# Optimization experiments

Hardware: AMD Instinct MI355X
Metric: run time of the kernel (lower is better)

Reference implementation:

```python
import jax, jax.numpy as jnp
import numpy as np

N_HEAD = 16


def setup_inputs() -> dict:
    key = jax.random.key(0)
    ks = jax.random.split(key, 5)
    B, T, C = 4, 2048, 1024
    s = 0.02
    x = jax.random.normal(ks[0], (B, T, C), jnp.float32)
    wq = jax.random.normal(ks[1], (C, C), jnp.float32) * s
    wk = jax.random.normal(ks[2], (C, C), jnp.float32) * s
    wv = jax.random.normal(ks[3], (C, C), jnp.float32) * s
    wp = jax.random.normal(ks[4], (C, C), jnp.float32) * s
    zb = jnp.zeros((C,), jnp.float32)
    return {"x": x, "wq": wq, "bq": zb, "wk": wk, "bk": zb,
            "wv": wv, "bv": zb, "wp": wp, "bp": zb}


def _rope_cos_sin(T, D):
    half = D // 2
    i = jnp.arange(half, dtype=jnp.float32)
    alpha = 1.0 / (10000.0 ** (2.0 * i / D))        # [half]
    ang = jnp.arange(T, dtype=jnp.float32)[:, None] * alpha  # [T, half]
    return jnp.cos(ang), jnp.sin(ang)


def _apply_rope(t, cos, sin):
    # t: [B, H, T, D]; non-interleaved halves as in the torch module
    half = t.shape[-1] // 2
    xr, xi = t[..., :half], t[..., half:]
    return jnp.concatenate([xr * cos - xi * sin, xr * sin + xi * cos], axis=-1)


def reference(x, wq, bq, wk, bk, wv, bv, wp, bp):
    B, T, C = x.shape
    H = N_HEAD
    D = C // H
    # QKV projections (torch Linear: x @ W.T + b)
    def heads(w, b):
        return (x @ w.T + b).reshape(B, T, H, D).transpose(0, 2, 1, 3)
    q, k, v = heads(wq, bq), heads(wk, bk), heads(wv, bv)
    cos, sin = _rope_cos_sin(T, D)  # each [T, D//2], broadcasts over B,H
    q = _apply_rope(q, cos, sin)
    k = _apply_rope(k, cos, sin)
    scale = 1.0 / np.sqrt(D).astype(np.float32)
    att = jnp.einsum('bhtd,bhsd->bhts', q, k) * scale  # [B,H,T,T]
    causal = jnp.tril(jnp.ones((T, T), bool))
    att = jnp.where(causal, att, jnp.float32(-jnp.inf))
    att = jax.nn.softmax(att, axis=-1)
    y = jnp.einsum('bhts,bhsd->bhtd', att, v)  # [B,H,T,D]
    y = y.transpose(0, 2, 1, 3).reshape(B, T, C)
    return y @ wp.T + bp
```

## Files before the change

kernel.cpp:

```cpp
#include <hip/hip_runtime.h>
#include <math.h>

constexpr int B = 4, T = 2048, C = 1024, H = 16, D = 64;
constexpr int M = B * T;
constexpr size_t BTC = (size_t)B * T * C;

typedef short bf16x8 __attribute__((ext_vector_type(8)));
typedef float f32x4 __attribute__((ext_vector_type(4)));

__device__ inline ushort f2bf(float f) {
  union { float f; unsigned u; } cv; cv.f = f;
  unsigned u = cv.u;
  u += 0x7fffu + ((u >> 16) & 1u);
  return (ushort)(u >> 16);
}
__device__ inline ushort f2bfr(float f) {
  union { float f; unsigned u; } cv; cv.f = f;
  return (ushort)((cv.u + 0x8000u) >> 16);
}
__device__ inline float bf2f(ushort u) {
  union { unsigned u; float f; } cv; cv.u = ((unsigned)u) << 16; return cv.f;
}

__device__ inline void async_load16(const void* g, void* l) {
  __builtin_amdgcn_global_load_lds(
      (const __attribute__((address_space(1))) void*)g,
      (__attribute__((address_space(3))) void*)l, 16, 0, 0);
}

__device__ __forceinline__ bf16x8 ones_frag() {
  bf16x8 v;
#pragma unroll
  for (int i = 0; i < 8; i++) v[i] = (short)0x3F80;
  return v;
}

__global__ __launch_bounds__(256) void f32_to_bf16(
    const float* __restrict__ in, ushort* __restrict__ outp) {
  int i = (blockIdx.x * 256 + threadIdx.x) * 4;
  float4 v = *(const float4*)(in + i);
  ushort4 o;
  o.x = f2bf(v.x); o.y = f2bf(v.y); o.z = f2bf(v.z); o.w = f2bf(v.w);
  *(ushort4*)(outp + i) = o;
}

__global__ __launch_bounds__(256) void conv_weights(
    const float* __restrict__ w0, const float* __restrict__ w1,
    const float* __restrict__ w2, const float* __restrict__ w3,
    ushort* __restrict__ outp) {
  const int seg_blocks = (C * C) / 1024;
  int seg = blockIdx.x / seg_blocks;
  int blk = blockIdx.x - seg * seg_blocks;
  const float* src = (seg == 0) ? w0 : (seg == 1) ? w1 : (seg == 2) ? w2 : w3;
  int i = (blk * 256 + threadIdx.x) * 4;
  float4 v = *(const float4*)(src + i);
  ushort4 o;
  o.x = f2bf(v.x); o.y = f2bf(v.y); o.z = f2bf(v.z); o.w = f2bf(v.w);
  *(ushort4*)(outp + (size_t)seg * C * C + i) = o;
}

#define GT 128
#define GBK 64
template <bool BF16OUT>
__global__ __launch_bounds__(256) void gemm_mfma_bt(
    const ushort* __restrict__ A, const ushort* __restrict__ Wt,
    const float* __restrict__ b0, const float* __restrict__ b1,
    const float* __restrict__ b2, void* __restrict__ outp,
    int N, int K) {
  __shared__ ushort As[GT * GBK] __attribute__((aligned(16)));
  __shared__ ushort Bs[GT * GBK] __attribute__((aligned(16)));
  int tid = threadIdx.x;
  int lane = tid & 63;
  int lrow = lane & 15, quad = lane >> 4;
  int wave = tid >> 6;
  int wr = wave >> 1, wc = wave & 1;
  int row0 = blockIdx.y * GT;
  int col0 = blockIdx.x * GT;
  const float* bias = (col0 < 1024) ? b0 : (col0 < 2048) ? b1 : b2;

  size_t ga[4], gb[4];
#pragma unroll
  for (int i = 0; i < 4; i++) {
    int cc = tid + i * 256;
    int r = cc >> 3, cl = cc & 7;
    int g = (cl ^ (r & 7)) * 8;
    ga[i] = (size_t)(row0 + r) * K + g;
    gb[i] = (size_t)(col0 + r) * K + g;
  }
  int x7 = lrow & 7;

  f32x4 acc[4][4];
#pragma unroll
  for (int i = 0; i < 4; i++)
#pragma unroll
    for (int j = 0; j < 4; j++) acc[i][j] = (f32x4){0.f, 0.f, 0.f, 0.f};

  for (int k0 = 0; k0 < K; k0 += GBK) {
#pragma unroll
    for (int i = 0; i < 4; i++) {
      int cc = tid + i * 256;
      async_load16(A + ga[i] + k0, &As[cc * 8]);
      async_load16(Wt + gb[i] + k0, &Bs[cc * 8]);
    }
    __syncthreads();
#pragma unroll
    for (int kh = 0; kh < 2; kh++) {
      int slot = ((kh * 4 + quad) ^ x7) * 8;
      bf16x8 af[4], bfr[4];
#pragma unroll
      for (int i = 0; i < 4; i++)
        af[i] = *(const bf16x8*)&As[(wr * 64 + i * 16 + lrow) * GBK + slot];
#pragma unroll
      for (int j = 0; j < 4; j++)
        bfr[j] = *(const bf16x8*)&Bs[(wc * 64 + j * 16 + lrow) * GBK + slot];
#pragma unroll
      for (int i = 0; i < 4; i++)
#pragma unroll
        for (int j = 0; j < 4; j++)
          acc[i][j] = __builtin_amdgcn_mfma_f32_16x16x32_bf16(af[i], bfr[j], acc[i][j], 0, 0, 0);
    }
    __syncthreads();
  }

#pragma unroll
  for (int i = 0; i < 4; i++)
#pragma unroll
    for (int j = 0; j < 4; j++) {
      int n = col0 + wc * 64 + j * 16 + lrow;
      float bn = bias[n & 1023];
#pragma unroll
      for (int r = 0; r < 4; r++) {
        int m = row0 + wr * 64 + i * 16 + quad * 4 + r;
        float v = acc[i][j][r] + bn;
        if (BF16OUT) ((ushort*)outp)[(size_t)m * N + n] = f2bf(v);
        else         ((float*)outp)[(size_t)m * N + n] = v;
      }
    }
}

__global__ __launch_bounds__(256) void rope_transpose_qk(
    const ushort* __restrict__ qkv, ushort* __restrict__ qout,
    ushort* __restrict__ kout) {
  int idx = blockIdx.x * blockDim.x + threadIdx.x;
  int i = idx & 31;
  int t = (idx >> 5) & (T - 1);
  int h = (idx >> 16) & (H - 1);
  int b = idx >> 20;
  int isK = blockIdx.y;
  const ushort* src = qkv + ((size_t)b * T + t) * (3 * C) + isK * C + h * D;
  float scale = isK ? 1.0f : 0.18033688011112042f;
  float xr = bf2f(src[i]);
  float xi = bf2f(src[i + 32]);
  float alpha = __builtin_amdgcn_exp2f((float)i * -0.415241011861f);
  float ang = (float)t * alpha;
  float c, s;
  __sincosf(ang, &s, &c);
  ushort* dst = (isK ? kout : qout) + (((size_t)b * H + h) * T + t) * D;
  dst[i]      = f2bf((xr * c - xi * s) * scale);
  dst[i + 32] = f2bf((xr * s + xi * c) * scale);
}

__global__ __launch_bounds__(256) void transpose_vt(
    const ushort* __restrict__ in, ushort* __restrict__ outp) {
  __shared__ ushort tile[64][65];
  int bh = blockIdx.y;
  int b = bh >> 4, h = bh & 15;
  int t0 = blockIdx.x * 64;
#pragma unroll
  for (int i = 0; i < 16; i++) {
    int lin = threadIdx.x + i * 256;
    int d = lin & 63, tq = lin >> 6;
    tile[d][tq] = in[((size_t)b * T + t0 + tq) * (3 * C) + h * D + d];
  }
  __syncthreads();
#pragma unroll
  for (int i = 0; i < 16; i++) {
    int lin = threadIdx.x + i * 256;
    int tq = lin & 63, d = lin >> 6;
    outp[((size_t)bh * D + d) * T + t0 + tq] = tile[d][tq];
  }
}

__device__ __forceinline__ void stage_kv(
    const ushort* kbh, const ushort* vbh, int s0,
    ushort* Kl, ushort* Vl, int tid) {
#pragma unroll
  for (int i = 0; i < 2; i++) {
    int c = tid + i * 256;
    int r = c >> 3, cc = c & 7;
    int g = (cc ^ (r & 7)) * 8;
    async_load16(kbh + (size_t)(s0 + r) * D + g, Kl + c * 8);
    async_load16(vbh + (size_t)r * T + s0 + g, Vl + c * 8);
  }
}

template <int MODE>
__device__ __forceinline__ void attn_step4(
    int s0, const ushort* KL, const ushort* VL, ushort* P,
    const bf16x8 (&qf)[2][2], int lrow, int quad, int sw0, int sw1,
    int qg0, int qg1, f32x4 (&o)[4][2], f32x4 (&ol)[2]) {
  bf16x8 kf0[4], kf1[4];
#pragma unroll
  for (int kt = 0; kt < 4; kt++) {
    int base = (kt * 16 + lrow) * 64;
    kf0[kt] = *(const bf16x8*)&KL[base + sw0];
    kf1[kt] = *(const bf16x8*)&KL[base + sw1];
  }
  bf16x8 vf0[4], vf1[4];
#pragma unroll
  for (int ds = 0; ds < 4; ds++) {
    int base = (ds * 16 + lrow) * 64;
    vf0[ds] = *(const bf16x8*)&VL[base + sw0];
    vf1[ds] = *(const bf16x8*)&VL[base + sw1];
  }
#pragma unroll
  for (int g = 0; g < 2; g++) {
    if (MODE == 2 && g == 0) continue;
    int qg = g ? qg1 : qg0;
    f32x4 st[4];
#pragma unroll
    for (int kt = 0; kt < 4; kt++) {
      f32x4 z = {0.f, 0.f, 0.f, 0.f};
      st[kt] = __builtin_amdgcn_mfma_f32_16x16x32_bf16(kf0[kt], qf[g][0], z, 0, 0, 0);
      st[kt] = __builtin_amdgcn_mfma_f32_16x16x32_bf16(kf1[kt], qf[g][1], st[kt], 0, 0, 0);
    }
    if ((MODE == 1 && g == 0) || (MODE == 2 && g == 1)) {
#pragma unroll
      for (int kt = 0; kt < 4; kt++)
#pragma unroll
        for (int r = 0; r < 4; r++)
          if (s0 + kt * 16 + quad * 4 + r > qg) st[kt][r] = -1e30f;
    }
#pragma unroll
    for (int kt = 0; kt < 4; kt++) {
      ushort4 pk;
      pk.x = f2bfr(__builtin_amdgcn_exp2f(st[kt][0]));
      pk.y = f2bfr(__builtin_amdgcn_exp2f(st[kt][1]));
      pk.z = f2bfr(__builtin_amdgcn_exp2f(st[kt][2]));
      pk.w = f2bfr(__builtin_amdgcn_exp2f(st[kt][3]));
      *(ushort4*)&P[((2 * kt + (quad >> 1)) * 32 + g * 16 + lrow) * 8 + (quad & 1) * 4] = pk;
    }
  }
  asm volatile("" ::: "memory");
  bf16x8 ones = ones_frag();
#pragma unroll
  for (int g = 0; g < 2; g++) {
    if (MODE == 2 && g == 0) continue;
    bf16x8 pf0 = *(const bf16x8*)&P[(quad * 32 + g * 16 + lrow) * 8];
    bf16x8 pf1 = *(const bf16x8*)&P[((quad + 4) * 32 + g * 16 + lrow) * 8];
    ol[g] = __builtin_amdgcn_mfma_f32_16x16x32_bf16(ones, pf0, ol[g], 0, 0, 0);
    ol[g] = __builtin_amdgcn_mfma_f32_16x16x32_bf16(ones, pf1, ol[g], 0, 0, 0);
#pragma unroll
    for (int ds = 0; ds < 4; ds++) {
      o[ds][g] = __builtin_amdgcn_mfma_f32_16x16x32_bf16(vf0[ds], pf0, o[ds][g], 0, 0, 0);
      o[ds][g] = __builtin_amdgcn_mfma_f32_16x16x32_bf16(vf1[ds], pf1, o[ds][g], 0, 0, 0);
    }
  }
}

__global__ __launch_bounds__(256, 3) void attn_mfma4(
    const ushort* __restrict__ qb_, const ushort* __restrict__ kb_,
    const ushort* __restrict__ vtb_, ushort* __restrict__ y) {
  __shared__ ushort Kl[2][64 * 64] __attribute__((aligned(16)));
  __shared__ ushort Vl[2][64 * 64] __attribute__((aligned(16)));
  __shared__ ushort Pl[4][2048] __attribute__((aligned(16)));
  int tid = threadIdx.x;
  int wave = tid >> 6, lane = tid & 63;
  int lrow = lane & 15, quad = lane >> 4;
  int qbi = 15 - (int)(blockIdx.x >> 6);
  int bh = blockIdx.x & 63;
  int b = bh >> 4, h = bh & 15;
  int Q0 = qbi * 128;
  ushort* P = Pl[wave];
  const ushort* kbh = kb_ + (size_t)bh * T * D;
  const ushort* vbh = vtb_ + (size_t)bh * D * T;

  int qg0 = Q0 + wave * 16 + lrow;
  int qg1 = qg0 + 64;
  bf16x8 qf[2][2];
  {
    const ushort* qp0 = qb_ + ((size_t)bh * T + qg0) * D + quad * 8;
    qf[0][0] = *(const bf16x8*)qp0;
    qf[0][1] = *(const bf16x8*)(qp0 + 32);
    const ushort* qp1 = qb_ + ((size_t)bh * T + qg1) * D + quad * 8;
    qf[1][0] = *(const bf16x8*)qp1;
    qf[1][1] = *(const bf16x8*)(qp1 + 32);
  }
  int r7 = lrow & 7;
  int sw0 = (quad ^ r7) * 8;
  int sw1 = ((quad + 4) ^ r7) * 8;

  f32x4 o[4][2];
#pragma unroll
  for (int ds = 0; ds < 4; ds++)
#pragma unroll
    for (int g = 0; g < 2; g++) o[ds][g] = (f32x4){0.f, 0.f, 0.f, 0.f};
  f32x4 ol[2] = {(f32x4){0.f, 0.f, 0.f, 0.f}, (f32x4){0.f, 0.f, 0.f, 0.f}};

  int trips = 2 * qbi + 2;
  stage_kv(kbh, vbh, 0, Kl[0], Vl[0], tid);
  int it = 0;
  for (; it < trips - 2; ++it) {
    __syncthreads();
    stage_kv(kbh, vbh, (it + 1) * 64, Kl[(it + 1) & 1], Vl[(it + 1) & 1], tid);
    attn_step4<0>(it * 64, Kl[it & 1], Vl[it & 1], P, qf, lrow, quad, sw0, sw1,
                  qg0, qg1, o, ol);
  }
  __syncthreads();
  stage_kv(kbh, vbh, (it + 1) * 64, Kl[(it + 1) & 1], Vl[(it + 1) & 1], tid);
  attn_step4<1>(it * 64, Kl[it & 1], Vl[it & 1], P, qf, lrow, quad, sw0, sw1,
                qg0, qg1, o, ol);
  ++it;
  __syncthreads();
  attn_step4<2>(it * 64, Kl[it & 1], Vl[it & 1], P, qf, lrow, quad, sw0, sw1,
                qg0, qg1, o, ol);

#pragma unroll
  for (int g = 0; g < 2; g++) {
    float inv = 1.f / ol[g][0];
    int qg = g ? qg1 : qg0;
#pragma unroll
    for (int ds = 0; ds < 4; ds++) {
      ushort4 pk;
      pk.x = f2bf(o[ds][g][0] * inv);
      pk.y = f2bf(o[ds][g][1] * inv);
      pk.z = f2bf(o[ds][g][2] * inv);
      pk.w = f2bf(o[ds][g][3] * inv);
      *(ushort4*)(y + ((size_t)b * T + qg) * C + h * D + ds * 16 + quad * 4) = pk;
    }
  }
}

extern "C" void kernel_launch(void* const* d_in, const int* in_sizes, int n_in,
                              void* d_out, int out_size, void* d_ws, size_t ws_size,
                              hipStream_t stream) {
  const float* x  = (const float*)d_in[0];
  const float* wq = (const float*)d_in[1];
  const float* bq = (const float*)d_in[2];
  const float* wk = (const float*)d_in[3];
  const float* bk = (const float*)d_in[4];
  const float* wv = (const float*)d_in[5];
  const float* bv = (const float*)d_in[6];
  const float* wp = (const float*)d_in[7];
  const float* bp = (const float*)d_in[8];
  float* out = (float*)d_out;

  ushort* xb    = (ushort*)d_ws;
  ushort* qkvb  = xb + BTC;
  ushort* qb    = qkvb + 3 * BTC;
  ushort* kb    = qb + BTC;
  ushort* vtb   = kb + BTC;
  ushort* wqkvb = vtb + BTC;
  ushort* wpb   = wqkvb + (size_t)3 * C * C;

  f32_to_bf16<<<(int)(BTC / 1024), 256, 0, stream>>>(x, xb);
  conv_weights<<<4 * (C * C) / 1024, 256, 0, stream>>>(wq, wk, wv, wp, wqkvb);

  dim3 qkv_grid(3 * C / GT, M / GT);
  gemm_mfma_bt<true><<<qkv_grid, 256, 0, stream>>>(
      xb, wqkvb, bq, bk, bv, qkvb, 3 * C, C);

  dim3 rope_grid((B * H * T * 32) / 256, 2);
  rope_transpose_qk<<<rope_grid, 256, 0, stream>>>(qkvb, qb, kb);
  dim3 vt_grid(T / 64, B * H);
  transpose_vt<<<vt_grid, 256, 0, stream>>>(qkvb + 2 * C, vtb);

  attn_mfma4<<<(B * H * T / 128), 256, 0, stream>>>(qb, kb, vtb, qkvb);

  dim3 proj_grid(C / GT, M / GT);
  gemm_mfma_bt<false><<<proj_grid, 256, 0, stream>>>(
      qkvb, wpb, bp, bp, bp, out, C, C);
}
```

Baseline: 263.6 us.

## Fuse RoPE, head transpose and V transpose into QKV GEMM epilogue

The QKV projection GEMM epilogue now applies RoPE and the Q scale and writes Q and K straight into [B,H,T,D] layout. It also writes V transposed into [B,H,D,T], so the separate rope_transpose_qk and transpose_vt kernels and the intermediate qkv buffer are gone. This removes two kernel launches and a full round trip of the 3*B*T*C bf16 intermediate through global memory. In exchange the epilogue does sincos per element and its stores are more scattered and less coalesced, for example 2-byte strided writes into the per-head layouts.

```diff
diff --git a/kernel.cpp b/kernel.cpp
--- a/kernel.cpp
+++ b/kernel.cpp
@@ -4,6 +4,8 @@
 constexpr int B = 4, T = 2048, C = 1024, H = 16, D = 64;
 constexpr int M = B * T;
 constexpr size_t BTC = (size_t)B * T * C;
+constexpr float QSCALE = 0.18033688011112042f;
+constexpr float ROPE_C = -0.415241011861f;
 
 typedef short bf16x8 __attribute__((ext_vector_type(8)));
 typedef float f32x4 __attribute__((ext_vector_type(4)));
@@ -17,9 +19,6 @@
 __device__ inline ushort f2bfr(float f) {
   union { float f; unsigned u; } cv; cv.f = f;
   return (ushort)((cv.u + 0x8000u) >> 16);
-}
-__device__ inline float bf2f(ushort u) {
-  union { unsigned u; float f; } cv; cv.u = ((unsigned)u) << 16; return cv.f;
 }
 
 __device__ inline void async_load16(const void* g, void* l) {
@@ -61,11 +60,12 @@
 
 #define GT 128
 #define GBK 64
-template <bool BF16OUT>
+template <int OM>
 __global__ __launch_bounds__(256) void gemm_mfma_bt(
     const ushort* __restrict__ A, const ushort* __restrict__ Wt,
     const float* __restrict__ b0, const float* __restrict__ b1,
-    const float* __restrict__ b2, void* __restrict__ outp,
+    const float* __restrict__ b2, void* __restrict__ out1,
+    void* __restrict__ out2, void* __restrict__ out3,
     int N, int K) {
   __shared__ ushort As[GT * GBK] __attribute__((aligned(16)));
   __shared__ ushort Bs[GT * GBK] __attribute__((aligned(16)));
@@ -122,62 +122,72 @@
     __syncthreads();
   }
 
-#pragma unroll
-  for (int i = 0; i < 4; i++)
-#pragma unroll
-    for (int j = 0; j < 4; j++) {
-      int n = col0 + wc * 64 + j * 16 + lrow;
-      float bn = bias[n & 1023];
-#pragma unroll
-      for (int r = 0; r < 4; r++) {
-        int m = row0 + wr * 64 + i * 16 + quad * 4 + r;
-        float v = acc[i][j][r] + bn;
-        if (BF16OUT) ((ushort*)outp)[(size_t)m * N + n] = f2bf(v);
-        else         ((float*)outp)[(size_t)m * N + n] = v;
+  int nb = col0 + wc * 64;
+  int mbase = row0 + wr * 64;
+  float bn[4];
+#pragma unroll
+  for (int j = 0; j < 4; j++) bn[j] = bias[(nb & 1023) + j * 16 + lrow];
+
+  if (OM == 0) {
+    float* outp = (float*)out1;
+#pragma unroll
+    for (int i = 0; i < 4; i++)
+#pragma unroll
+      for (int j = 0; j < 4; j++) {
+        int n = nb + j * 16 + lrow;
+#pragma unroll
+        for (int r = 0; r < 4; r++) {
+          int m = mbase + i * 16 + quad * 4 + r;
+          outp[(size_t)m * N + n] = acc[i][j][r] + bn[j];
+        }
       }
-    }
-}
-
-__global__ __launch_bounds__(256) void rope_transpose_qk(
-    const ushort* __restrict__ qkv, ushort* __restrict__ qout,
-    ushort* __restrict__ kout) {
-  int idx = blockIdx.x * blockDim.x + threadIdx.x;
-  int i = idx & 31;
-  int t = (idx >> 5) & (T - 1);
-  int h = (idx >> 16) & (H - 1);
-  int b = idx >> 20;
-  int isK = blockIdx.y;
-  const ushort* src = qkv + ((size_t)b * T + t) * (3 * C) + isK * C + h * D;
-  float scale = isK ? 1.0f : 0.18033688011112042f;
-  float xr = bf2f(src[i]);
-  float xi = bf2f(src[i + 32]);
-  float alpha = __builtin_amdgcn_exp2f((float)i * -0.415241011861f);
-  float ang = (float)t * alpha;
-  float c, s;
-  __sincosf(ang, &s, &c);
-  ushort* dst = (isK ? kout : qout) + (((size_t)b * H + h) * T + t) * D;
-  dst[i]      = f2bf((xr * c - xi * s) * scale);
-  dst[i + 32] = f2bf((xr * s + xi * c) * scale);
-}
-
-__global__ __launch_bounds__(256) void transpose_vt(
-    const ushort* __restrict__ in, ushort* __restrict__ outp) {
-  __shared__ ushort tile[64][65];
-  int bh = blockIdx.y;
-  int b = bh >> 4, h = bh & 15;
-  int t0 = blockIdx.x * 64;
-#pragma unroll
-  for (int i = 0; i < 16; i++) {
-    int lin = threadIdx.x + i * 256;
-    int d = lin & 63, tq = lin >> 6;
-    tile[d][tq] = in[((size_t)b * T + t0 + tq) * (3 * C) + h * D + d];
-  }
-  __syncthreads();
-#pragma unroll
-  for (int i = 0; i < 16; i++) {
-    int lin = threadIdx.x + i * 256;
-    int tq = lin & 63, d = lin >> 6;
-    outp[((size_t)bh * D + d) * T + t0 + tq] = tile[d][tq];
+  } else {
+    int seg = nb >> 10;
+    int hh = (nb & 1023) >> 6;
+    if (seg < 2) {
+      ushort* dst = (seg == 0) ? (ushort*)out1 : (ushort*)out2;
+      float scale = (seg == 0) ? QSCALE : 1.0f;
+      float a0 = __builtin_amdgcn_exp2f((float)lrow * ROPE_C);
+      float a1 = __builtin_amdgcn_exp2f((float)(lrow + 16) * ROPE_C);
+#pragma unroll
+      for (int i = 0; i < 4; i++) {
+#pragma unroll
+        for (int r = 0; r < 4; r++) {
+          int m = mbase + i * 16 + quad * 4 + r;
+          int t = m & (T - 1), bb = m >> 11;
+          float s0, c0, s1, c1;
+          __sincosf((float)t * a0, &s0, &c0);
+          __sincosf((float)t * a1, &s1, &c1);
+          float xr0 = acc[i][0][r] + bn[0];
+          float xi0 = acc[i][2][r] + bn[2];
+          float xr1 = acc[i][1][r] + bn[1];
+          float xi1 = acc[i][3][r] + bn[3];
+          ushort* p = dst + ((size_t)(bb * H + hh) * T + t) * D + lrow;
+          p[0]  = f2bf((xr0 * c0 - xi0 * s0) * scale);
+          p[32] = f2bf((xr0 * s0 + xi0 * c0) * scale);
+          p[16] = f2bf((xr1 * c1 - xi1 * s1) * scale);
+          p[48] = f2bf((xr1 * s1 + xi1 * c1) * scale);
+        }
+      }
+    } else {
+      ushort* dst = (ushort*)out3;
+#pragma unroll
+      for (int i = 0; i < 4; i++) {
+        int m0 = mbase + i * 16 + quad * 4;
+        int t0 = m0 & (T - 1), bb = m0 >> 11;
+        size_t base = (size_t)(bb * H + hh) * D * T + t0;
+#pragma unroll
+        for (int j = 0; j < 4; j++) {
+          int d = j * 16 + lrow;
+          ushort4 pk;
+          pk.x = f2bf(acc[i][j][0] + bn[j]);
+          pk.y = f2bf(acc[i][j][1] + bn[j]);
+          pk.z = f2bf(acc[i][j][2] + bn[j]);
+          pk.w = f2bf(acc[i][j][3] + bn[j]);
+          *(ushort4*)(dst + base + (size_t)d * T) = pk;
+        }
+      }
+    }
   }
 }
 
@@ -346,28 +356,23 @@
   float* out = (float*)d_out;
 
   ushort* xb    = (ushort*)d_ws;
-  ushort* qkvb  = xb + BTC;
-  ushort* qb    = qkvb + 3 * BTC;
+  ushort* qb    = xb + BTC;
   ushort* kb    = qb + BTC;
   ushort* vtb   = kb + BTC;
-  ushort* wqkvb = vtb + BTC;
+  ushort* yb    = vtb + BTC;
+  ushort* wqkvb = yb + BTC;
   ushort* wpb   = wqkvb + (size_t)3 * C * C;
 
   f32_to_bf16<<<(int)(BTC / 1024), 256, 0, stream>>>(x, xb);
   conv_weights<<<4 * (C * C) / 1024, 256, 0, stream>>>(wq, wk, wv, wp, wqkvb);
 
   dim3 qkv_grid(3 * C / GT, M / GT);
-  gemm_mfma_bt<true><<<qkv_grid, 256, 0, stream>>>(
-      xb, wqkvb, bq, bk, bv, qkvb, 3 * C, C);
-
-  dim3 rope_grid((B * H * T * 32) / 256, 2);
-  rope_transpose_qk<<<rope_grid, 256, 0, stream>>>(qkvb, qb, kb);
-  dim3 vt_grid(T / 64, B * H);
-  transpose_vt<<<vt_grid, 256, 0, stream>>>(qkvb + 2 * C, vtb);
-
-  attn_mfma4<<<(B * H * T / 128), 256, 0, stream>>>(qb, kb, vtb, qkvb);
+  gemm_mfma_bt<1><<<qkv_grid, 256, 0, stream>>>(
+      xb, wqkvb, bq, bk, bv, qb, kb, vtb, 3 * C, C);
+
+  attn_mfma4<<<(B * H * T / 128), 256, 0, stream>>>(qb, kb, vtb, yb);
 
   dim3 proj_grid(C / GT, M / GT);
-  gemm_mfma_bt<false><<<proj_grid, 256, 0, stream>>>(
-      qkvb, wpb, bp, bp, bp, out, C, C);
-}
+  gemm_mfma_bt<0><<<proj_grid, 256, 0, stream>>>(
+      yb, wpb, bp, bp, bp, out, nullptr, nullptr, C, C);
+}
```

Result: faster. 246.8 us (-6.3%).
